# Performance work log

Hardware: AMD Instinct MI355X
Metric: run time of the kernel (lower is better)

Reference implementation:

```python
import jax, jax.numpy as jnp
import numpy as np

N_HEAD = 16
HEAD_DIM = 128  # n_embd // n_head
EPS = 1e-6
ROPE_BASE = 10000.0


def rmsnorm(x, w):
    rms = jnp.mean(x * x, axis=-1, keepdims=True)
    return w * (x * jax.lax.rsqrt(rms + EPS))


def rope_cache(T, head_dim):
    half = head_dim // 2
    inv_freq = 1.0 / (ROPE_BASE ** (jnp.arange(half, dtype=jnp.float32) / half))
    pos = jnp.arange(T, dtype=jnp.float32)
    freqs = pos[:, None] * inv_freq[None, :]  # [T, half]
    return jnp.cos(freqs), jnp.sin(freqs)


def apply_rope(x, cos, sin):
    # x: [B, H, T, D]; cos/sin: [T, D/2]
    half = x.shape[-1] // 2
    x1, x2 = x[..., :half], x[..., half:]
    return jnp.concatenate([x1 * cos - x2 * sin, x1 * sin + x2 * cos], axis=-1)


def setup_inputs() -> dict:
    key = jax.random.key(0)
    ks = jax.random.split(key, 8)
    B, T, C, Hid = 2, 2048, 2048, 5632
    s = 0.02
    return {
        "x": jax.random.normal(ks[0], (B, T, C), dtype=jnp.float32),
        "w_norm1": jnp.ones((C,), dtype=jnp.float32),
        "w_qkv": jax.random.normal(ks[1], (C, 3 * C), dtype=jnp.float32) * s,
        "w_proj": jax.random.normal(ks[2], (C, C), dtype=jnp.float32) * s,
        "w_norm2": jnp.ones((C,), dtype=jnp.float32),
        "w1": jax.random.normal(ks[3], (C, Hid), dtype=jnp.float32) * s,
        "w2": jax.random.normal(ks[4], (C, Hid), dtype=jnp.float32) * s,
        "w3": jax.random.normal(ks[5], (Hid, C), dtype=jnp.float32) * s,
    }


def reference(x, w_norm1, w_qkv, w_proj, w_norm2, w1, w2, w3):
    B, T, C = x.shape
    H, D = N_HEAD, HEAD_DIM

    # ---- attention branch ----
    h = rmsnorm(x, w_norm1)
    qkv = h @ w_qkv  # [B, T, 3C]
    q, k, v = jnp.split(qkv, 3, axis=-1)
    q = q.reshape(B, T, H, D).transpose(0, 2, 1, 3)  # [B,H,T,D]
    k = k.reshape(B, T, H, D).transpose(0, 2, 1, 3)
    v = v.reshape(B, T, H, D).transpose(0, 2, 1, 3)

    cos, sin = rope_cache(T, D)
    q = apply_rope(q, cos, sin)
    k = apply_rope(k, cos, sin)

    att = jnp.einsum('bhqd,bhkd->bhqk', q, k) / np.sqrt(D).astype(np.float32)
    causal = jnp.tril(jnp.ones((T, T), dtype=bool))
    att = jnp.where(causal, att, -jnp.inf)
    att = jax.nn.softmax(att, axis=-1)
    out = jnp.einsum('bhqk,bhkd->bhqd', att, v)
    out = out.transpose(0, 2, 1, 3).reshape(B, T, C)
    x = x + out @ w_proj

    # ---- SwiGLU MLP branch ----
    h2 = rmsnorm(x, w_norm2)
    x = x + (jax.nn.silu(h2 @ w1) * (h2 @ w2)) @ w3
    return x
```

## Files before the change

### kernel.cpp

```cpp
#include <hip/hip_runtime.h>

typedef short s16x8 __attribute__((ext_vector_type(8)));
typedef unsigned short u16;
typedef u16 u16x8 __attribute__((ext_vector_type(8)));
typedef u16 u16x4 __attribute__((ext_vector_type(4)));
typedef float f32x4 __attribute__((ext_vector_type(4)));

#define DEVINL __device__ __forceinline__

DEVINL u16 f2bf(float f) {
    unsigned u = __float_as_uint(f);
    u += 0x7FFFu + ((u >> 16) & 1u);
    return (u16)(u >> 16);
}
DEVINL float bf2f(u16 h) { return __uint_as_float((unsigned)h << 16); }

DEVINL void gl2lds16(const void* g, void* l) {
    __builtin_amdgcn_global_load_lds((const __attribute__((address_space(1))) void*)g,
                                     (__attribute__((address_space(3))) void*)l, 16, 0, 0);
}

__global__ __launch_bounds__(256) void tcast(
    const float* __restrict__ src, u16* __restrict__ dst, const int K, const int N)
{
    __shared__ float tile[32][33];
    const long k0 = (long)blockIdx.x * 32;
    const long n0 = (long)blockIdx.y * 32;
    const int tid = threadIdx.x;
    const int r = tid >> 3, c4 = (tid & 7) * 4;
    float4 v = *(const float4*)&src[(k0 + r) * N + n0 + c4];
    tile[r][c4] = v.x; tile[r][c4 + 1] = v.y; tile[r][c4 + 2] = v.z; tile[r][c4 + 3] = v.w;
    __syncthreads();
    u16x4 ov;
    ov[0] = f2bf(tile[c4][r]);     ov[1] = f2bf(tile[c4 + 1][r]);
    ov[2] = f2bf(tile[c4 + 2][r]); ov[3] = f2bf(tile[c4 + 3][r]);
    *(u16x4*)&dst[(n0 + r) * K + k0 + c4] = ov;
}

__global__ __launch_bounds__(256) void rmsnorm_cast(
    const float* __restrict__ x, const float* __restrict__ wn, u16* __restrict__ out)
{
    const int C = 2048;
    const long row = blockIdx.x;
    const int tid = threadIdx.x;
    const float4* xr = (const float4*)(x + row * C);
    float4 a = xr[tid * 2], b = xr[tid * 2 + 1];
    float ss = a.x*a.x + a.y*a.y + a.z*a.z + a.w*a.w
             + b.x*b.x + b.y*b.y + b.z*b.z + b.w*b.w;
#pragma unroll
    for (int m = 1; m < 64; m <<= 1) ss += __shfl_xor(ss, m);
    __shared__ float red[4];
    if ((tid & 63) == 0) red[tid >> 6] = ss;
    __syncthreads();
    float scale = rsqrtf((red[0] + red[1] + red[2] + red[3]) * (1.f / 2048.f) + 1e-6f);
    const float4* wr = (const float4*)wn;
    float4 wa = wr[tid * 2], wb = wr[tid * 2 + 1];
    u16x8 o;
    o[0] = f2bf(a.x * scale * wa.x); o[1] = f2bf(a.y * scale * wa.y);
    o[2] = f2bf(a.z * scale * wa.z); o[3] = f2bf(a.w * scale * wa.w);
    o[4] = f2bf(b.x * scale * wb.x); o[5] = f2bf(b.y * scale * wb.y);
    o[6] = f2bf(b.z * scale * wb.z); o[7] = f2bf(b.w * scale * wb.w);
    *(u16x8*)&out[row * C + tid * 8] = o;
}

template <int MODE>
__global__ __launch_bounds__(256, 2) void gemm128(
    const u16* __restrict__ A, const u16* __restrict__ Bt,
    const int N, const int K,
    float* __restrict__ outF, u16* __restrict__ outB,
    const float* __restrict__ resid)
{
    __shared__ u16 As[128 * 64];
    __shared__ u16 Bs[128 * 64];
    const int tid = threadIdx.x;
    const int lane = tid & 63;
    const int w = tid >> 6;
    const int wm = w >> 1, wn = w & 1;
    const int quad = lane >> 4, l16 = lane & 15;
    const long m0 = (long)blockIdx.x * 128;
    const long n0 = (long)blockIdx.y * 128;

    const u16* ga[4]; const u16* gb[4]; char* la[4]; char* lb[4];
#pragma unroll
    for (int rr = 0; rr < 4; ++rr) {
        int idx = rr * 256 + tid;
        int r = idx >> 3, j = idx & 7;
        int c = (j ^ (r & 7)) * 8;
        ga[rr] = A + (m0 + r) * K + c;
        gb[rr] = Bt + (n0 + r) * K + c;
        la[rr] = (char*)As + idx * 16;
        lb[rr] = (char*)Bs + idx * 16;
    }

    f32x4 acc[4][4] = {};

    for (int k0 = 0; k0 < K; k0 += 64) {
#pragma unroll
        for (int rr = 0; rr < 4; ++rr) {
            gl2lds16(ga[rr] + k0, la[rr]);
            gl2lds16(gb[rr] + k0, lb[rr]);
        }
        __syncthreads();
#pragma unroll
        for (int ks = 0; ks < 2; ++ks) {
            s16x8 af[4], bfv[4];
#pragma unroll
            for (int mt = 0; mt < 4; ++mt)
                af[mt] = *(const s16x8*)&As[(wm * 64 + mt * 16 + l16) * 64 +
                                            ((ks * 4 + quad) ^ (l16 & 7)) * 8];
#pragma unroll
            for (int nt = 0; nt < 4; ++nt)
                bfv[nt] = *(const s16x8*)&Bs[(wn * 64 + nt * 16 + l16) * 64 +
                                             ((ks * 4 + quad) ^ (l16 & 7)) * 8];
#pragma unroll
            for (int mt = 0; mt < 4; ++mt)
#pragma unroll
                for (int nt = 0; nt < 4; ++nt)
                    acc[mt][nt] = __builtin_amdgcn_mfma_f32_16x16x32_bf16(af[mt], bfv[nt], acc[mt][nt], 0, 0, 0);
        }
        __syncthreads();
    }

#pragma unroll
    for (int mt = 0; mt < 4; ++mt)
#pragma unroll
        for (int reg = 0; reg < 4; ++reg) {
            long row = m0 + wm * 64 + mt * 16 + quad * 4 + reg;
#pragma unroll
            for (int nt = 0; nt < 4; ++nt) {
                long col = n0 + wn * 64 + nt * 16 + l16;
                float v = acc[mt][nt][reg];
                if (MODE == 0) {
                    outB[row * N + col] = f2bf(v);
                } else {
                    outF[row * N + col] = resid[row * N + col] + v;
                }
            }
        }
}

__global__ __launch_bounds__(256, 2) void gemm_ffn(
    const u16* __restrict__ A, const u16* __restrict__ B1t, const u16* __restrict__ B2t,
    const int N, const int K, u16* __restrict__ outB)
{
    __shared__ u16 As[128 * 64];
    __shared__ u16 B1s[128 * 64];
    __shared__ u16 B2s[128 * 64];
    const int tid = threadIdx.x;
    const int lane = tid & 63;
    const int w = tid >> 6;
    const int wm = w >> 1, wn = w & 1;
    const int quad = lane >> 4, l16 = lane & 15;
    const long m0 = (long)blockIdx.x * 128;
    const long n0 = (long)blockIdx.y * 128;

    const u16* ga[4]; const u16* gb1[4]; const u16* gb2[4];
    char* la[4]; char* lb1[4]; char* lb2[4];
#pragma unroll
    for (int rr = 0; rr < 4; ++rr) {
        int idx = rr * 256 + tid;
        int r = idx >> 3, j = idx & 7;
        int c = (j ^ (r & 7)) * 8;
        ga[rr]  = A + (m0 + r) * K + c;
        gb1[rr] = B1t + (n0 + r) * K + c;
        gb2[rr] = B2t + (n0 + r) * K + c;
        la[rr]  = (char*)As + idx * 16;
        lb1[rr] = (char*)B1s + idx * 16;
        lb2[rr] = (char*)B2s + idx * 16;
    }

    f32x4 acc1[4][4] = {};
    f32x4 acc2[4][4] = {};

    for (int k0 = 0; k0 < K; k0 += 64) {
#pragma unroll
        for (int rr = 0; rr < 4; ++rr) {
            gl2lds16(ga[rr] + k0, la[rr]);
            gl2lds16(gb1[rr] + k0, lb1[rr]);
            gl2lds16(gb2[rr] + k0, lb2[rr]);
        }
        __syncthreads();
#pragma unroll
        for (int ks = 0; ks < 2; ++ks) {
            s16x8 af[4], b1f[4], b2f[4];
#pragma unroll
            for (int mt = 0; mt < 4; ++mt)
                af[mt] = *(const s16x8*)&As[(wm * 64 + mt * 16 + l16) * 64 +
                                            ((ks * 4 + quad) ^ (l16 & 7)) * 8];
#pragma unroll
            for (int nt = 0; nt < 4; ++nt) {
                b1f[nt] = *(const s16x8*)&B1s[(wn * 64 + nt * 16 + l16) * 64 +
                                              ((ks * 4 + quad) ^ (l16 & 7)) * 8];
                b2f[nt] = *(const s16x8*)&B2s[(wn * 64 + nt * 16 + l16) * 64 +
                                              ((ks * 4 + quad) ^ (l16 & 7)) * 8];
            }
#pragma unroll
            for (int mt = 0; mt < 4; ++mt)
#pragma unroll
                for (int nt = 0; nt < 4; ++nt) {
                    acc1[mt][nt] = __builtin_amdgcn_mfma_f32_16x16x32_bf16(af[mt], b1f[nt], acc1[mt][nt], 0, 0, 0);
                    acc2[mt][nt] = __builtin_amdgcn_mfma_f32_16x16x32_bf16(af[mt], b2f[nt], acc2[mt][nt], 0, 0, 0);
                }
        }
        __syncthreads();
    }

#pragma unroll
    for (int mt = 0; mt < 4; ++mt)
#pragma unroll
        for (int reg = 0; reg < 4; ++reg) {
            long row = m0 + wm * 64 + mt * 16 + quad * 4 + reg;
#pragma unroll
            for (int nt = 0; nt < 4; ++nt) {
                long col = n0 + wn * 64 + nt * 16 + l16;
                float g = acc1[mt][nt][reg];
                float s = g / (1.f + __expf(-g));
                outB[row * N + col] = f2bf(s * acc2[mt][nt][reg]);
            }
        }
}

__global__ __launch_bounds__(256) void rope_qk(
    const u16* __restrict__ qkv, u16* __restrict__ qT, u16* __restrict__ kT)
{
    const int row = blockIdx.x;
    const int t = row & 2047, b = row >> 11;
    const int tid = threadIdx.x;
    __shared__ u16 buf[4096];
    const u16* src = qkv + (long)row * 6144;
    u16x8 aa = *(const u16x8*)&src[tid * 8];
    u16x8 kk = *(const u16x8*)&src[2048 + tid * 8];
    *(u16x8*)&buf[tid * 8] = aa;
    *(u16x8*)&buf[2048 + tid * 8] = kk;
    __syncthreads();
    const int c = tid * 8;
    const int h = c >> 7, dh = c & 127;
    const bool first = dh < 64;
    const int pc = first ? (c + 64) : (c - 64);
    float cs[8], sn[8];
#pragma unroll
    for (int j = 0; j < 8; ++j) {
        float inv = __expf(-(float)((dh & 63) + j) * 0.14391156831212787f);
        float ang = (float)t * inv;
        cs[j] = cosf(ang); sn[j] = sinf(ang);
    }
    const long obase = ((long)(b * 16 + h) * 2048 + t) * 128 + dh;
#pragma unroll
    for (int part = 0; part < 2; ++part) {
        const int base = part * 2048;
        u16x8 mine = *(const u16x8*)&buf[base + c];
        u16x8 oth  = *(const u16x8*)&buf[base + pc];
        const float qs = part ? 1.f : 0.08838834764831845f;
        u16x8 o;
#pragma unroll
        for (int j = 0; j < 8; ++j) {
            float xv = bf2f(mine[j]), yv = bf2f(oth[j]);
            float ov = first ? (xv * cs[j] - yv * sn[j]) : (yv * sn[j] + xv * cs[j]);
            o[j] = f2bf(ov * qs);
        }
        u16* dst = part ? kT : qT;
        *(u16x8*)&dst[obase] = o;
    }
}

__global__ __launch_bounds__(256) void vtrans(
    const u16* __restrict__ qkv, u16* __restrict__ vT)
{
    const int bh = blockIdx.x;
    const int b = bh >> 4, h = bh & 15;
    const int t0 = blockIdx.y * 64, d0 = blockIdx.z * 64;
    __shared__ u16 tile[64 * 65];
    const int tid = threadIdx.x;
#pragma unroll
    for (int rr = 0; rr < 2; ++rr) {
        int idx = rr * 256 + tid;
        int r = idx >> 3, c = (idx & 7) * 8;
        u16x8 v = *(const u16x8*)&qkv[(long)(b * 2048 + t0 + r) * 6144 + 4096 + h * 128 + d0 + c];
#pragma unroll
        for (int j = 0; j < 8; ++j) tile[r * 65 + c + j] = v[j];
    }
    __syncthreads();
#pragma unroll
    for (int rr = 0; rr < 2; ++rr) {
        int idx = rr * 256 + tid;
        int dd = idx >> 3, cc = (idx & 7) * 8;
        u16x8 o;
#pragma unroll
        for (int j = 0; j < 8; ++j) o[j] = tile[(cc + j) * 65 + dd];
        *(u16x8*)&vT[((long)bh * 128 + d0 + dd) * 2048 + t0 + cc] = o;
    }
}

__global__ __launch_bounds__(256, 2) void attn_kernel(
    const u16* __restrict__ qT, const u16* __restrict__ kT,
    const u16* __restrict__ vT, u16* __restrict__ outT)
{
    const int T = 2048, D = 128;
    const int lid = blockIdx.x;
    const int swz = (lid & 7) * 128 + (lid >> 3);
    const int bh = swz >> 5;
    const int qt = 31 - (swz & 31);
    const int tid = threadIdx.x, lane = tid & 63, w = tid >> 6;
    const int quad = lane >> 4, l16 = lane & 15;
    const int qrow = qt * 64 + w * 16;

    __shared__ u16 Ks[2][64 * 128];
    __shared__ u16 Vs[2][128 * 64];
    __shared__ u16 Ps[4][16 * 64];

    s16x8 aq[4];
    const u16* qb = qT + ((long)bh * T + qrow + l16) * D;
#pragma unroll
    for (int kk = 0; kk < 4; ++kk)
        aq[kk] = *(const s16x8*)&qb[kk * 32 + quad * 8];

    f32x4 o[8] = {};
    float mi[4] = {-INFINITY, -INFINITY, -INFINITY, -INFINITY};
    float li[4] = {0.f, 0.f, 0.f, 0.f};

    const u16* kg0 = kT + (long)bh * T * D;
    const u16* vg0 = vT + (long)bh * D * T;

    auto stage = [&](int kt, int b) {
        const int k0 = kt * 64;
#pragma unroll
        for (int rr = 0; rr < 4; ++rr) {
            int idx = rr * 256 + tid;
            int kr = idx >> 4, kj = idx & 15;
            gl2lds16(kg0 + (long)(k0 + kr) * D + ((kj ^ (kr & 15)) * 8),
                     (char*)Ks[b] + idx * 16);
            int vr = idx >> 3, vj = idx & 7;
            gl2lds16(vg0 + (long)vr * T + k0 + ((vj ^ (vr & 7)) * 8),
                     (char*)Vs[b] + idx * 16);
        }
    };

    stage(0, 0);

    for (int kt = 0; kt <= qt; ++kt) {
        __syncthreads();
        if (kt < qt) stage(kt + 1, (kt + 1) & 1);
        const u16* ks_ = Ks[kt & 1];
        const u16* vs_ = Vs[kt & 1];
        const int k0 = kt * 64;

        f32x4 sf[4] = {};
        __builtin_amdgcn_s_setprio(1);
#pragma unroll
        for (int kk = 0; kk < 4; ++kk) {
#pragma unroll
            for (int nt = 0; nt < 4; ++nt) {
                s16x8 kb = *(const s16x8*)&ks_[(nt * 16 + l16) * 128 +
                                               ((kk * 4 + quad) ^ (l16 & 15)) * 8];
                sf[nt] = __builtin_amdgcn_mfma_f32_16x16x32_bf16(aq[kk], kb, sf[nt], 0, 0, 0);
            }
        }
        __builtin_amdgcn_s_setprio(0);

        float S[4][4];
        if (kt == qt) {
#pragma unroll
            for (int nt = 0; nt < 4; ++nt) {
                int col = k0 + nt * 16 + l16;
#pragma unroll
                for (int reg = 0; reg < 4; ++reg) {
                    int row = qrow + quad * 4 + reg;
                    S[nt][reg] = (col <= row) ? sf[nt][reg] : -INFINITY;
                }
            }
        } else {
#pragma unroll
            for (int nt = 0; nt < 4; ++nt)
#pragma unroll
                for (int reg = 0; reg < 4; ++reg)
                    S[nt][reg] = sf[nt][reg];
        }

        float rm[4];
#pragma unroll
        for (int reg = 0; reg < 4; ++reg)
            rm[reg] = fmaxf(fmaxf(S[0][reg], S[1][reg]), fmaxf(S[2][reg], S[3][reg]));
#pragma unroll
        for (int m = 1; m < 16; m <<= 1)
#pragma unroll
            for (int reg = 0; reg < 4; ++reg)
                rm[reg] = fmaxf(rm[reg], __shfl_xor(rm[reg], m));

        int cond = 1;
#pragma unroll
        for (int reg = 0; reg < 4; ++reg)
            cond &= (rm[reg] - mi[reg] <= 8.f) ? 1 : 0;
        if (!__all(cond)) {
            float alpha[4];
#pragma unroll
            for (int reg = 0; reg < 4; ++reg) {
                float mn = fmaxf(mi[reg], rm[reg]);
                alpha[reg] = __expf(mi[reg] - mn);
                mi[reg] = mn;
                li[reg] *= alpha[reg];
            }
#pragma unroll
            for (int dt = 0; dt < 8; ++dt)
#pragma unroll
                for (int reg = 0; reg < 4; ++reg)
                    o[dt][reg] *= alpha[reg];
        }

        float rs[4] = {};
#pragma unroll
        for (int nt = 0; nt < 4; ++nt)
#pragma unroll
            for (int reg = 0; reg < 4; ++reg) {
                float p = __expf(S[nt][reg] - mi[reg]);
                S[nt][reg] = p;
                rs[reg] += p;
            }
#pragma unroll
        for (int m = 1; m < 16; m <<= 1)
#pragma unroll
            for (int reg = 0; reg < 4; ++reg)
                rs[reg] += __shfl_xor(rs[reg], m);
#pragma unroll
        for (int reg = 0; reg < 4; ++reg)
            li[reg] += rs[reg];

#pragma unroll
        for (int nt = 0; nt < 4; ++nt)
#pragma unroll
            for (int reg = 0; reg < 4; ++reg) {
                int prow = quad * 4 + reg;
                int pcol = nt * 16 + l16;
                Ps[w][prow * 64 + (((pcol >> 3) ^ (prow & 7)) * 8) + (pcol & 7)]
                    = f2bf(S[nt][reg]);
            }

        __builtin_amdgcn_s_setprio(1);
#pragma unroll
        for (int ks = 0; ks < 2; ++ks) {
            s16x8 pa = *(const s16x8*)&Ps[w][l16 * 64 +
                                             ((ks * 4 + quad) ^ (l16 & 7)) * 8];
#pragma unroll
            for (int dt = 0; dt < 8; ++dt) {
                s16x8 vb = *(const s16x8*)&vs_[(dt * 16 + l16) * 64 +
                                               ((ks * 4 + quad) ^ (l16 & 7)) * 8];
                o[dt] = __builtin_amdgcn_mfma_f32_16x16x32_bf16(pa, vb, o[dt], 0, 0, 0);
            }
        }
        __builtin_amdgcn_s_setprio(0);
    }

    const int b = bh >> 4, h = bh & 15;
#pragma unroll
    for (int reg = 0; reg < 4; ++reg) {
        float inv = 1.f / li[reg];
        int t = qrow + quad * 4 + reg;
        u16* orow = outT + ((long)(b * T + t)) * 2048 + h * 128;
#pragma unroll
        for (int dt = 0; dt < 8; ++dt)
            orow[dt * 16 + l16] = f2bf(o[dt][reg] * inv);
    }
}

extern "C" void kernel_launch(void* const* d_in, const int* in_sizes, int n_in,
                              void* d_out, int out_size, void* d_ws, size_t ws_size,
                              hipStream_t stream) {
    const float* x      = (const float*)d_in[0];
    const float* wn1    = (const float*)d_in[1];
    const float* w_qkv  = (const float*)d_in[2];
    const float* w_proj = (const float*)d_in[3];
    const float* wn2    = (const float*)d_in[4];
    const float* w1     = (const float*)d_in[5];
    const float* w2     = (const float*)d_in[6];
    const float* w3     = (const float*)d_in[7];
    float* out = (float*)d_out;

    char* p = (char*)d_ws;
    u16* Z       = (u16*)p; p += (size_t)6144 * 2048 * 2;
    u16* wproj_t = (u16*)p; p += (size_t)2048 * 2048 * 2;
    u16* w1_t    = (u16*)p; p += (size_t)5632 * 2048 * 2;
    u16* w2_t    = (u16*)p; p += (size_t)5632 * 2048 * 2;
    u16* C       = (u16*)p; p += (size_t)4096 * 2048 * 2;
    u16* D       = (u16*)p; p += (size_t)4096 * 6144 * 2;
    u16* E       = (u16*)p; p += (size_t)3 * 32 * 2048 * 128 * 2;

    u16* wqkv_t = Z;
    u16* w3_t   = Z;
    u16* qT = E;
    u16* kT = E + (size_t)32 * 2048 * 128;
    u16* vT = E + (size_t)2 * 32 * 2048 * 128;
    float* x2 = (float*)E;
    u16* uu = D;

    tcast<<<dim3(64, 192), 256, 0, stream>>>(w_qkv, wqkv_t, 2048, 6144);
    tcast<<<dim3(64, 64), 256, 0, stream>>>(w_proj, wproj_t, 2048, 2048);
    tcast<<<dim3(64, 176), 256, 0, stream>>>(w1, w1_t, 2048, 5632);
    tcast<<<dim3(64, 176), 256, 0, stream>>>(w2, w2_t, 2048, 5632);

    rmsnorm_cast<<<4096, 256, 0, stream>>>(x, wn1, C);
    gemm128<0><<<dim3(32, 48), 256, 0, stream>>>(C, wqkv_t, 6144, 2048,
                                                 nullptr, D, nullptr);
    rope_qk<<<4096, 256, 0, stream>>>(D, qT, kT);
    vtrans<<<dim3(32, 32, 2), 256, 0, stream>>>(D, vT);

    tcast<<<dim3(176, 64), 256, 0, stream>>>(w3, w3_t, 5632, 2048);

    attn_kernel<<<1024, 256, 0, stream>>>(qT, kT, vT, C);

    gemm128<1><<<dim3(32, 16), 256, 0, stream>>>(C, wproj_t, 2048, 2048,
                                                 x2, nullptr, x);
    rmsnorm_cast<<<4096, 256, 0, stream>>>(x2, wn2, C);
    gemm_ffn<<<dim3(32, 44), 256, 0, stream>>>(C, w1_t, w2_t, 5632, 2048, uu);
    gemm128<1><<<dim3(32, 16), 256, 0, stream>>>(uu, w3_t, 2048, 5632,
                                                 out, nullptr, x2);
}
```

Measured before the change: 849.7 us.

## Give each wave a full 128-row tile strip in the GEMM kernels

The plain GEMM drops from 4 waves to 2 waves per block. Each wave now computes 128x64 with 32 accumulators, so the A fragments are read from shared memory once per wave and B is reused across eight M tiles. The FFN GEMM keeps 4 waves, but each wave now covers all 128 rows by 32 columns. The aim is to raise MFMA work per LDS read. In exchange, accumulator registers per thread roughly double, and the 128-thread blocks issue fewer loads in parallel, which may lower occupancy and latency hiding.

```diff
diff --git a/kernel.cpp b/kernel.cpp
--- a/kernel.cpp
+++ b/kernel.cpp
@@ -18,6 +18,10 @@
 DEVINL void gl2lds16(const void* g, void* l) {
     __builtin_amdgcn_global_load_lds((const __attribute__((address_space(1))) void*)g,
                                      (__attribute__((address_space(3))) void*)l, 16, 0, 0);
+}
+
+DEVINL f32x4 mfma16(s16x8 a, s16x8 b, f32x4 c) {
+    return __builtin_amdgcn_mfma_f32_16x16x32_bf16(a, b, c, 0, 0, 0);
 }
 
 __global__ __launch_bounds__(256) void tcast(
@@ -64,7 +68,7 @@
 }
 
 template <int MODE>
-__global__ __launch_bounds__(256, 2) void gemm128(
+__global__ __launch_bounds__(128, 2) void gemmW(
     const u16* __restrict__ A, const u16* __restrict__ Bt,
     const int N, const int K,
     float* __restrict__ outF, u16* __restrict__ outB,
@@ -75,61 +79,61 @@
     const int tid = threadIdx.x;
     const int lane = tid & 63;
     const int w = tid >> 6;
-    const int wm = w >> 1, wn = w & 1;
     const int quad = lane >> 4, l16 = lane & 15;
+    const int asw = l16 & 7;
     const long m0 = (long)blockIdx.x * 128;
     const long n0 = (long)blockIdx.y * 128;
 
-    const u16* ga[4]; const u16* gb[4]; char* la[4]; char* lb[4];
-#pragma unroll
-    for (int rr = 0; rr < 4; ++rr) {
-        int idx = rr * 256 + tid;
-        int r = idx >> 3, j = idx & 7;
-        int c = (j ^ (r & 7)) * 8;
-        ga[rr] = A + (m0 + r) * K + c;
-        gb[rr] = Bt + (n0 + r) * K + c;
-        la[rr] = (char*)As + idx * 16;
-        lb[rr] = (char*)Bs + idx * 16;
-    }
-
-    f32x4 acc[4][4] = {};
+    const int r0 = tid >> 3;
+    const int c0 = ((tid & 7) ^ (r0 & 7)) * 8;
+    const u16* gA = A + (m0 + r0) * K + c0;
+    const u16* gB = Bt + (n0 + r0) * K + c0;
+    char* lA = (char*)As + tid * 16;
+    char* lB = (char*)Bs + tid * 16;
+    const long rstep = (long)16 * K;
+
+    f32x4 acc[8][4] = {};
 
     for (int k0 = 0; k0 < K; k0 += 64) {
 #pragma unroll
-        for (int rr = 0; rr < 4; ++rr) {
-            gl2lds16(ga[rr] + k0, la[rr]);
-            gl2lds16(gb[rr] + k0, lb[rr]);
-        }
+        for (int rr = 0; rr < 8; ++rr)
+            gl2lds16(gA + k0 + rr * rstep, lA + rr * 2048);
+#pragma unroll
+        for (int rr = 0; rr < 8; ++rr)
+            gl2lds16(gB + k0 + rr * rstep, lB + rr * 2048);
         __syncthreads();
 #pragma unroll
         for (int ks = 0; ks < 2; ++ks) {
-            s16x8 af[4], bfv[4];
-#pragma unroll
-            for (int mt = 0; mt < 4; ++mt)
-                af[mt] = *(const s16x8*)&As[(wm * 64 + mt * 16 + l16) * 64 +
-                                            ((ks * 4 + quad) ^ (l16 & 7)) * 8];
+            const int csel = ((ks * 4 + quad) ^ asw) * 8;
+            s16x8 b[4];
 #pragma unroll
             for (int nt = 0; nt < 4; ++nt)
-                bfv[nt] = *(const s16x8*)&Bs[(wn * 64 + nt * 16 + l16) * 64 +
-                                             ((ks * 4 + quad) ^ (l16 & 7)) * 8];
-#pragma unroll
-            for (int mt = 0; mt < 4; ++mt)
-#pragma unroll
-                for (int nt = 0; nt < 4; ++nt)
-                    acc[mt][nt] = __builtin_amdgcn_mfma_f32_16x16x32_bf16(af[mt], bfv[nt], acc[mt][nt], 0, 0, 0);
+                b[nt] = *(const s16x8*)&Bs[(w * 64 + nt * 16 + l16) * 64 + csel];
+#pragma unroll
+            for (int mh = 0; mh < 2; ++mh) {
+                s16x8 a[4];
+#pragma unroll
+                for (int mt = 0; mt < 4; ++mt)
+                    a[mt] = *(const s16x8*)&As[((mh * 4 + mt) * 16 + l16) * 64 + csel];
+#pragma unroll
+                for (int mt = 0; mt < 4; ++mt)
+#pragma unroll
+                    for (int nt = 0; nt < 4; ++nt)
+                        acc[mh * 4 + mt][nt] = mfma16(a[mt], b[nt], acc[mh * 4 + mt][nt]);
+            }
         }
         __syncthreads();
     }
 
 #pragma unroll
-    for (int mt = 0; mt < 4; ++mt)
+    for (int mtg = 0; mtg < 8; ++mtg)
 #pragma unroll
         for (int reg = 0; reg < 4; ++reg) {
-            long row = m0 + wm * 64 + mt * 16 + quad * 4 + reg;
+            long row = m0 + mtg * 16 + quad * 4 + reg;
 #pragma unroll
             for (int nt = 0; nt < 4; ++nt) {
-                long col = n0 + wn * 64 + nt * 16 + l16;
-                float v = acc[mt][nt][reg];
+                long col = n0 + w * 64 + nt * 16 + l16;
+                float v = acc[mtg][nt][reg];
                 if (MODE == 0) {
                     outB[row * N + col] = f2bf(v);
                 } else {
@@ -139,7 +143,7 @@
         }
 }
 
-__global__ __launch_bounds__(256, 2) void gemm_ffn(
+__global__ __launch_bounds__(256, 2) void gemmFFNW(
     const u16* __restrict__ A, const u16* __restrict__ B1t, const u16* __restrict__ B2t,
     const int N, const int K, u16* __restrict__ outB)
 {
@@ -149,73 +153,73 @@
     const int tid = threadIdx.x;
     const int lane = tid & 63;
     const int w = tid >> 6;
-    const int wm = w >> 1, wn = w & 1;
     const int quad = lane >> 4, l16 = lane & 15;
+    const int asw = l16 & 7;
     const long m0 = (long)blockIdx.x * 128;
     const long n0 = (long)blockIdx.y * 128;
 
-    const u16* ga[4]; const u16* gb1[4]; const u16* gb2[4];
-    char* la[4]; char* lb1[4]; char* lb2[4];
-#pragma unroll
-    for (int rr = 0; rr < 4; ++rr) {
-        int idx = rr * 256 + tid;
-        int r = idx >> 3, j = idx & 7;
-        int c = (j ^ (r & 7)) * 8;
-        ga[rr]  = A + (m0 + r) * K + c;
-        gb1[rr] = B1t + (n0 + r) * K + c;
-        gb2[rr] = B2t + (n0 + r) * K + c;
-        la[rr]  = (char*)As + idx * 16;
-        lb1[rr] = (char*)B1s + idx * 16;
-        lb2[rr] = (char*)B2s + idx * 16;
-    }
-
-    f32x4 acc1[4][4] = {};
-    f32x4 acc2[4][4] = {};
+    const int r0 = tid >> 3;
+    const int c0 = ((tid & 7) ^ (r0 & 7)) * 8;
+    const u16* gA  = A   + (m0 + r0) * K + c0;
+    const u16* gB1 = B1t + (n0 + r0) * K + c0;
+    const u16* gB2 = B2t + (n0 + r0) * K + c0;
+    char* lA  = (char*)As  + tid * 16;
+    char* lB1 = (char*)B1s + tid * 16;
+    char* lB2 = (char*)B2s + tid * 16;
+    const long rstep = (long)32 * K;
+
+    f32x4 acc1[8][2] = {};
+    f32x4 acc2[8][2] = {};
 
     for (int k0 = 0; k0 < K; k0 += 64) {
 #pragma unroll
-        for (int rr = 0; rr < 4; ++rr) {
-            gl2lds16(ga[rr] + k0, la[rr]);
-            gl2lds16(gb1[rr] + k0, lb1[rr]);
-            gl2lds16(gb2[rr] + k0, lb2[rr]);
-        }
+        for (int rr = 0; rr < 4; ++rr)
+            gl2lds16(gA + k0 + rr * rstep, lA + rr * 4096);
+#pragma unroll
+        for (int rr = 0; rr < 4; ++rr)
+            gl2lds16(gB1 + k0 + rr * rstep, lB1 + rr * 4096);
+#pragma unroll
+        for (int rr = 0; rr < 4; ++rr)
+            gl2lds16(gB2 + k0 + rr * rstep, lB2 + rr * 4096);
         __syncthreads();
 #pragma unroll
         for (int ks = 0; ks < 2; ++ks) {
-            s16x8 af[4], b1f[4], b2f[4];
-#pragma unroll
-            for (int mt = 0; mt < 4; ++mt)
-                af[mt] = *(const s16x8*)&As[(wm * 64 + mt * 16 + l16) * 64 +
-                                            ((ks * 4 + quad) ^ (l16 & 7)) * 8];
-#pragma unroll
-            for (int nt = 0; nt < 4; ++nt) {
-                b1f[nt] = *(const s16x8*)&B1s[(wn * 64 + nt * 16 + l16) * 64 +
-                                              ((ks * 4 + quad) ^ (l16 & 7)) * 8];
-                b2f[nt] = *(const s16x8*)&B2s[(wn * 64 + nt * 16 + l16) * 64 +
-                                              ((ks * 4 + quad) ^ (l16 & 7)) * 8];
-            }
-#pragma unroll
-            for (int mt = 0; mt < 4; ++mt)
-#pragma unroll
-                for (int nt = 0; nt < 4; ++nt) {
-                    acc1[mt][nt] = __builtin_amdgcn_mfma_f32_16x16x32_bf16(af[mt], b1f[nt], acc1[mt][nt], 0, 0, 0);
-                    acc2[mt][nt] = __builtin_amdgcn_mfma_f32_16x16x32_bf16(af[mt], b2f[nt], acc2[mt][nt], 0, 0, 0);
-                }
+            const int csel = ((ks * 4 + quad) ^ asw) * 8;
+            s16x8 b1[2], b2[2];
+#pragma unroll
+            for (int nt = 0; nt < 2; ++nt) {
+                b1[nt] = *(const s16x8*)&B1s[(w * 32 + nt * 16 + l16) * 64 + csel];
+                b2[nt] = *(const s16x8*)&B2s[(w * 32 + nt * 16 + l16) * 64 + csel];
+            }
+#pragma unroll
+            for (int mh = 0; mh < 2; ++mh) {
+                s16x8 a[4];
+#pragma unroll
+                for (int mt = 0; mt < 4; ++mt)
+                    a[mt] = *(const s16x8*)&As[((mh * 4 + mt) * 16 + l16) * 64 + csel];
+#pragma unroll
+                for (int mt = 0; mt < 4; ++mt)
+#pragma unroll
+                    for (int nt = 0; nt < 2; ++nt) {
+                        acc1[mh * 4 + mt][nt] = mfma16(a[mt], b1[nt], acc1[mh * 4 + mt][nt]);
+                        acc2[mh * 4 + mt][nt] = mfma16(a[mt], b2[nt], acc2[mh * 4 + mt][nt]);
+                    }
+            }
         }
         __syncthreads();
     }
 
 #pragma unroll
-    for (int mt = 0; mt < 4; ++mt)
+    for (int mtg = 0; mtg < 8; ++mtg)
 #pragma unroll
         for (int reg = 0; reg < 4; ++reg) {
-            long row = m0 + wm * 64 + mt * 16 + quad * 4 + reg;
-#pragma unroll
-            for (int nt = 0; nt < 4; ++nt) {
-                long col = n0 + wn * 64 + nt * 16 + l16;
-                float g = acc1[mt][nt][reg];
+            long row = m0 + mtg * 16 + quad * 4 + reg;
+#pragma unroll
+            for (int nt = 0; nt < 2; ++nt) {
+                long col = n0 + w * 32 + nt * 16 + l16;
+                float g = acc1[mtg][nt][reg];
                 float s = g / (1.f + __expf(-g));
-                outB[row * N + col] = f2bf(s * acc2[mt][nt][reg]);
+                outB[row * N + col] = f2bf(s * acc2[mtg][nt][reg]);
             }
         }
 }
@@ -497,8 +501,8 @@
     tcast<<<dim3(64, 176), 256, 0, stream>>>(w2, w2_t, 2048, 5632);
 
     rmsnorm_cast<<<4096, 256, 0, stream>>>(x, wn1, C);
-    gemm128<0><<<dim3(32, 48), 256, 0, stream>>>(C, wqkv_t, 6144, 2048,
-                                                 nullptr, D, nullptr);
+    gemmW<0><<<dim3(32, 48), 128, 0, stream>>>(C, wqkv_t, 6144, 2048,
+                                               nullptr, D, nullptr);
     rope_qk<<<4096, 256, 0, stream>>>(D, qT, kT);
     vtrans<<<dim3(32, 32, 2), 256, 0, stream>>>(D, vT);
 
@@ -506,10 +510,10 @@
 
     attn_kernel<<<1024, 256, 0, stream>>>(qT, kT, vT, C);
 
-    gemm128<1><<<dim3(32, 16), 256, 0, stream>>>(C, wproj_t, 2048, 2048,
-                                                 x2, nullptr, x);
+    gemmW<1><<<dim3(32, 16), 128, 0, stream>>>(C, wproj_t, 2048, 2048,
+                                               x2, nullptr, x);
     rmsnorm_cast<<<4096, 256, 0, stream>>>(x2, wn2, C);
-    gemm_ffn<<<dim3(32, 44), 256, 0, stream>>>(C, w1_t, w2_t, 5632, 2048, uu);
-    gemm128<1><<<dim3(32, 16), 256, 0, stream>>>(uu, w3_t, 2048, 5632,
-                                                 out, nullptr, x2);
-}
+    gemmFFNW<<<dim3(32, 44), 256, 0, stream>>>(C, w1_t, w2_t, 5632, 2048, uu);
+    gemmW<1><<<dim3(32, 16), 128, 0, stream>>>(uu, w3_t, 2048, 5632,
+                                               out, nullptr, x2);
+}
```

Measured after the change: 886.7 us. 1.04x slower.
